# Performance work log

Measured on AMD Instinct MI355X. Metric: run time of the kernel, lower is better.

Reference implementation:

```python
import jax, jax.numpy as jnp
import numpy as np

N = 100000
CTX = 128
TGT = 32
H = 64
FUS = H + H // 2  # 96
E1 = 1600000
E2 = 800000
LN_EPS = 1e-5


def _gelu(x):
    return jax.nn.gelu(x, approximate=False)  # torch default is exact erf GELU


def _layer_norm(x, g, b):
    mu = jnp.mean(x, -1, keepdims=True)
    xc = x - mu
    var = jnp.mean(xc * xc, -1, keepdims=True)
    return xc * jax.lax.rsqrt(var + LN_EPS) * g + b


def _gcn_conv(x, W, b, ei, n):
    # PyG GCNConv: x' = D^-1/2 (A + I) D^-1/2 (x W) + b, with unit edge weights.
    h = x @ W  # [N, out]
    src, dst = ei[0], ei[1]
    deg = jnp.zeros((n,), h.dtype).at[dst].add(1.0) + 1.0  # +1 for self-loop
    dinv = jax.lax.rsqrt(deg)
    norm = dinv[src] * dinv[dst]  # [E]
    agg = jnp.zeros_like(h).at[dst].add(h[src] * norm[:, None])
    agg = agg + h * (dinv * dinv)[:, None]  # self-loop messages
    return agg + b


def setup_inputs() -> dict:
    key = jax.random.key(0)
    ks = jax.random.split(key, 32)
    def lin(k, fan_in, fan_out):
        s = 1.0 / np.sqrt(fan_in)
        k1, k2 = jax.random.split(k)
        return (jax.random.uniform(k1, (fan_in, fan_out), jnp.float32, -s, s),
                jax.random.uniform(k2, (fan_out,), jnp.float32, -s, s))
    inp = {}
    inp['context'] = jax.random.normal(ks[0], (N, CTX), jnp.float32)
    inp['target'] = jax.random.normal(ks[1], (N, TGT), jnp.float32)
    inp['mask'] = jax.random.bernoulli(ks[2], 0.5, (N, TGT))
    inp['adj_ei'] = jax.random.randint(ks[3], (2, E1), 0, N, jnp.int64 if jax.config.jax_enable_x64 else jnp.int32)
    inp['transit_ei'] = jax.random.randint(ks[4], (2, E2), 0, N, jnp.int64 if jax.config.jax_enable_x64 else jnp.int32)
    inp['mask_token'] = jax.random.normal(ks[5], (1, TGT), jnp.float32) * 0.01
    inp['ce_W1'], inp['ce_b1'] = lin(ks[6], CTX, H)
    inp['ce_g'] = jnp.ones((H,), jnp.float32)
    inp['ce_beta'] = jnp.zeros((H,), jnp.float32)
    inp['ce_W2'], inp['ce_b2'] = lin(ks[7], H, H)
    inp['te_W'], inp['te_b'] = lin(ks[8], TGT, H // 2)
    inp['g1_W'], inp['g1_b'] = lin(ks[9], FUS, H)
    inp['g2_W'], inp['g2_b'] = lin(ks[10], H, H)
    inp['t1_W'], inp['t1_b'] = lin(ks[11], FUS, H)
    inp['t2_W'], inp['t2_b'] = lin(ks[12], H, H)
    inp['alpha'] = jnp.float32(0.5)
    inp['h_W1'], inp['h_b1'] = lin(ks[13], H + FUS, H)
    inp['h_g'] = jnp.ones((H,), jnp.float32)
    inp['h_beta'] = jnp.zeros((H,), jnp.float32)
    inp['h_W2'], inp['h_b2'] = lin(ks[14], H, TGT)
    return inp


def reference(context, target, mask, adj_ei, transit_ei, mask_token,
              ce_W1, ce_b1, ce_g, ce_beta, ce_W2, ce_b2,
              te_W, te_b,
              g1_W, g1_b, g2_W, g2_b,
              t1_W, t1_b, t2_W, t2_b,
              alpha,
              h_W1, h_b1, h_g, h_beta, h_W2, h_b2):
    n = context.shape[0]
    # context encoder (eval mode: dropout is identity)
    c = _gelu(_layer_norm(context @ ce_W1 + ce_b1, ce_g, ce_beta))
    ctx = _gelu(c @ ce_W2 + ce_b2)
    # masked target encoder
    m = mask.astype(target.dtype)
    masked_t = target * (1.0 - m) + mask_token * m
    tgt = _gelu(masked_t @ te_W + te_b)
    fused = jnp.concatenate([ctx, tgt], -1)  # [N, 96]
    # spatial branch
    h1 = _gelu(_gcn_conv(fused, g1_W, g1_b, adj_ei, n))
    h_sp = _gcn_conv(h1, g2_W, g2_b, adj_ei, n)
    # transit branch
    h2 = _gelu(_gcn_conv(fused, t1_W, t1_b, transit_ei, n))
    h_tr = _gcn_conv(h2, t2_W, t2_b, transit_ei, n)
    a = jax.nn.sigmoid(alpha)
    h = a * h_sp + (1.0 - a) * h_tr
    z = jnp.concatenate([h, fused], -1)  # [N, 160]
    z = _gelu(_layer_norm(z @ h_W1 + h_b1, h_g, h_beta))
    return z @ h_W2 + h_b2  # [N, 32]
```

## Files before the change

kernel.cpp:

```cpp
#include <hip/hip_runtime.h>
#include <math.h>


#define LN_EPS 1e-5f
#define NRANGES 512
#define RMASK 511
#define LSHIFT 9
#define PASSP_EDGES 8192
#define GSTRIDE 16

typedef __attribute__((ext_vector_type(8))) short short8;
typedef __attribute__((ext_vector_type(4))) float float4v;
typedef __attribute__((ext_vector_type(4))) unsigned short ushort4v;

__device__ __forceinline__ float gelu_exact(float x) {
    return 0.5f * x * (1.0f + erff(x * 0.70710678118654752440f));
}

__device__ __forceinline__ float qsum16(float v) {
#pragma unroll
    for (int m = 1; m < 16; m <<= 1)
        v += __shfl_xor(v, m, 64);
    return v;
}

__device__ __forceinline__ int load_edge(const void* ei, int is32, long idx) {
    return is32 ? ((const int*)ei)[idx] : (int)((const long long*)ei)[idx];
}

__device__ __forceinline__ unsigned short f32_to_bf16(float f) {
    unsigned int x = __float_as_uint(f);
    x += 0x7fffu + ((x >> 16) & 1u);
    return (unsigned short)(x >> 16);
}
__device__ __forceinline__ float bf16_to_f32(unsigned short u) {
    return __uint_as_float((unsigned int)u << 16);
}
__device__ __forceinline__ float bflo(unsigned x) { return __uint_as_float(x << 16); }
__device__ __forceinline__ float bfhi(unsigned x) { return __uint_as_float(x & 0xffff0000u); }

__device__ __forceinline__ void load_dst4(const void* ei1, int e1, const void* ei2, int e2,
                                          int n, int is32, int base, int nv, int nd[4]) {
    if (is32 && nv == 4) {
        if (base + 3 < e1 && (((e1 + base) & 3) == 0)) {
            int4 v = *(const int4*)((const int*)ei1 + (size_t)e1 + base);
            nd[0] = v.x; nd[1] = v.y; nd[2] = v.z; nd[3] = v.w;
            return;
        }
        if (base >= e1 && (((e2 + base - e1) & 3) == 0)) {
            int4 v = *(const int4*)((const int*)ei2 + (size_t)e2 + (base - e1));
            nd[0] = v.x + n; nd[1] = v.y + n; nd[2] = v.z + n; nd[3] = v.w + n;
            return;
        }
    }
#pragma unroll
    for (int u = 0; u < 4; ++u) {
        int i = base + u;
        if (u >= nv) { nd[u] = -1; continue; }
        if (i < e1) nd[u] = load_edge(ei1, is32, (long)e1 + i);
        else        nd[u] = load_edge(ei2, is32, (long)e2 + (i - e1)) + n;
    }
}

__device__ __forceinline__ void load_src4(const void* ei1, int e1, const void* ei2, int e2,
                                          int is32, int base, int nv, int ns[4]) {
    if (is32 && nv == 4) {
        if (base + 3 < e1 && ((base & 3) == 0)) {
            int4 v = *(const int4*)((const int*)ei1 + base);
            ns[0] = v.x; ns[1] = v.y; ns[2] = v.z; ns[3] = v.w;
            return;
        }
        if (base >= e1 && (((base - e1) & 3) == 0)) {
            int4 v = *(const int4*)((const int*)ei2 + (base - e1));
            ns[0] = v.x; ns[1] = v.y; ns[2] = v.z; ns[3] = v.w;
            return;
        }
    }
#pragma unroll
    for (int u = 0; u < 4; ++u) {
        int i = base + u;
        if (u >= nv) { ns[u] = 0; continue; }
        if (i < e1) ns[u] = load_edge(ei1, is32, i);
        else        ns[u] = load_edge(ei2, is32, (long)(i - e1));
    }
}

__global__ __launch_bounds__(256) void detect_kernel(const unsigned char* __restrict__ mask_bytes,
                                                     const int* __restrict__ ei_words,
                                                     int* __restrict__ flags,
                                                     int* __restrict__ gcur, int cap) {
    if (blockIdx.x == 0) {
        __shared__ int f0, f1;
        if (threadIdx.x == 0) { f0 = 0; f1 = 0; }
        __syncthreads();
        int i = threadIdx.x;
        if ((i & 3) != 0 && mask_bytes[i] != 0) f0 = 1;
        if (i < 64 && ei_words[2 * i + 1] != 0) f1 = 1;
        __syncthreads();
        if (threadIdx.x == 0) { flags[0] = f0; flags[1] = f1; }
    } else {
        int r = (blockIdx.x - 1) * 256 + threadIdx.x;
        if (r < NRANGES) gcur[r * GSTRIDE] = r * cap;
    }
}

__device__ __forceinline__ void passp_body(
    const void* ei1, int e1, const void* ei2, int e2,
    int n, const int* flags, int* gcur, int cap, unsigned* ebuf, int sbits, int bid)
{
    __shared__ int hist[NRANGES];
    __shared__ int base[NRANGES];
    const int E = e1 + e2;
    const int is32 = flags[1];
    const int b0 = bid * PASSP_EDGES;
    const int bend = (b0 + PASSP_EDGES < E) ? b0 + PASSP_EDGES : E;
    const int tid = threadIdx.x;

    for (int k = tid; k < NRANGES; k += 1024) hist[k] = 0;
    __syncthreads();

    int nd[8], rk[8];
#pragma unroll
    for (int j = 0; j < 2; ++j) {
        int bi = b0 + j * 4096 + tid * 4;
        int nv = bend - bi; nv = (nv < 0) ? 0 : (nv > 4 ? 4 : nv);
        load_dst4(ei1, e1, ei2, e2, n, is32, bi, nv, &nd[j * 4]);
#pragma unroll
        for (int u = 0; u < 4; ++u)
            if (u < nv) rk[j * 4 + u] = atomicAdd(&hist[nd[j * 4 + u] & RMASK], 1);
    }
    __syncthreads();

    for (int r = tid; r < NRANGES; r += 1024) {
        int c = hist[r];
        base[r] = c ? atomicAdd(&gcur[r * GSTRIDE], c) : 0;
    }
    __syncthreads();

#pragma unroll
    for (int j = 0; j < 2; ++j) {
        int bi = b0 + j * 4096 + tid * 4;
        int nv = bend - bi; nv = (nv < 0) ? 0 : (nv > 4 ? 4 : nv);
        int sv[4];
        load_src4(ei1, e1, ei2, e2, is32, bi, nv, sv);
#pragma unroll
        for (int u = 0; u < 4; ++u) {
            if (u < nv) {
                int d = nd[j * 4 + u];
                int r = d & RMASK;
                int pos = base[r] + rk[j * 4 + u];
                if (pos < (r + 1) * cap)
                    ebuf[pos] = (unsigned)sv[u] | ((unsigned)(d >> LSHIFT) << sbits);
            }
        }
    }
}

__device__ __forceinline__ void prep_body(
    const float* context, const float* target, const void* mask, const int* flags,
    const float* mask_token, const float* te_W, const float* te_b,
    unsigned short* ctxb, unsigned short* fused, int n, int bid)
{
    __shared__ float tbuf[128][32];
    int w = threadIdx.x >> 6;
    int j = threadIdx.x & 63;
    int r0 = __builtin_amdgcn_readfirstlane(bid * 128 + w * 8);
    if (r0 >= n) return;

    const float4* src = (const float4*)(context + (size_t)r0 * 128);
    ushort4v* dst = (ushort4v*)(ctxb + (size_t)r0 * 128);
#pragma unroll
    for (int p = 0; p < 4; ++p) {
        float4 v = src[p * 64 + j];
        ushort4v o;
        o.x = f32_to_bf16(v.x); o.y = f32_to_bf16(v.y);
        o.z = f32_to_bf16(v.z); o.w = f32_to_bf16(v.w);
        dst[p * 64 + j] = o;
    }

    int tr = j >> 5;
    int tj = j & 31;
#pragma unroll
    for (int rr = 0; rr < 4; ++rr) {
        int r = tr + rr * 2;
        long mi = (long)(r0 + r) * 32 + tj;
        int mraw = flags[0] ? (int)((const unsigned char*)mask)[mi]
                            : ((const int*)mask)[mi];
        float m = mraw ? 1.0f : 0.0f;
        tbuf[w * 8 + r][tj] = target[mi] * (1.0f - m) + mask_token[tj] * m;
    }

#pragma unroll
    for (int rr = 0; rr < 4; ++rr) {
        int r = tr + rr * 2;
        float y3 = te_b[tj];
#pragma unroll
        for (int k = 0; k < 32; ++k)
            y3 = fmaf(tbuf[w * 8 + r][k], te_W[k * 32 + tj], y3);
        fused[(long)(r0 + r) * 96 + 64 + tj] = f32_to_bf16(gelu_exact(y3));
    }
}

__global__ __launch_bounds__(1024) void passp_prep_kernel(
    const void* __restrict__ ei1, int e1, const void* __restrict__ ei2, int e2,
    int n, const int* __restrict__ flags, int* __restrict__ gcur, int cap,
    unsigned* __restrict__ ebuf, int sbits, int ppBlocks,
    const float* __restrict__ context, const float* __restrict__ target,
    const void* __restrict__ mask, const float* __restrict__ mask_token,
    const float* __restrict__ te_W, const float* __restrict__ te_b,
    unsigned short* __restrict__ ctxb, unsigned short* __restrict__ fused)
{
    if ((int)blockIdx.x < ppBlocks)
        passp_body(ei1, e1, ei2, e2, n, flags, gcur, cap, ebuf, sbits, blockIdx.x);
    else
        prep_body(context, target, mask, flags, mask_token, te_W, te_b,
                  ctxb, fused, n, blockIdx.x - ppBlocks);
}

__device__ __forceinline__ void rscan_body(const int* gcur, int cap,
                                           int* rstart, int* rowptr, int n2) {
    __shared__ int ws[256];
    int t = threadIdx.x;
    int i0 = 2 * t, i1 = 2 * t + 1;
    int a0 = gcur[i0 * GSTRIDE] - i0 * cap;
    int a1 = gcur[i1 * GSTRIDE] - i1 * cap;
    ws[t] = a0 + a1;
    __syncthreads();
    for (int off = 1; off < 256; off <<= 1) {
        int v = (t >= off) ? ws[t - off] : 0;
        __syncthreads();
        if (t >= off) ws[t] += v;
        __syncthreads();
    }
    int ex = t ? ws[t - 1] : 0;
    rstart[i0] = ex;
    rstart[i1] = ex + a0;
    if (t == 255) { rstart[NRANGES] = ws[255]; rowptr[n2] = ws[255]; }
}

__device__ __forceinline__ void mfma_ln_body(
    const unsigned short* x, const float* W, const float* bias, const float* g,
    const float* beta, unsigned short* y, int n, int bid, int nblk)
{
    constexpr int K = 128, KS = K / 32, STRIDE = K + 8;
    __shared__ __align__(16) unsigned short wt[64 * STRIDE];
    int n0 = threadIdx.x & 63;
    int kk = threadIdx.x >> 6;
    for (int k = kk; k < K; k += 4)
        wt[n0 * STRIDE + k] = f32_to_bf16(W[k * 64 + n0]);
    __syncthreads();

    int w = threadIdx.x >> 6;
    int lane = threadIdx.x & 63;
    int c = lane & 15;
    int q = lane >> 4;

    short8 bfrag[KS][4];
#pragma unroll
    for (int s = 0; s < KS; ++s)
#pragma unroll
        for (int nt = 0; nt < 4; ++nt)
            bfrag[s][nt] = *(const short8*)&wt[(nt * 16 + c) * STRIDE + s * 32 + q * 8];

    float bs[4], gs[4], be[4];
#pragma unroll
    for (int nt = 0; nt < 4; ++nt) {
        bs[nt] = bias[nt * 16 + c];
        gs[nt] = g[nt * 16 + c];
        be[nt] = beta[nt * 16 + c];
    }

    int T = n >> 4;
    int stride = nblk * 4;
    for (int t = __builtin_amdgcn_readfirstlane(bid * 4 + w); t < T; t += stride) {
        int r0 = t << 4;
        const unsigned short* xa = x + (size_t)(r0 + c) * K + q * 8;
        float4v acc[4] = {{0,0,0,0},{0,0,0,0},{0,0,0,0},{0,0,0,0}};
#pragma unroll
        for (int s = 0; s < KS; ++s) {
            short8 a = *(const short8*)(xa + s * 32);
#pragma unroll
            for (int nt = 0; nt < 4; ++nt)
                acc[nt] = __builtin_amdgcn_mfma_f32_16x16x32_bf16(a, bfrag[s][nt], acc[nt], 0, 0, 0);
        }
#pragma unroll
        for (int reg = 0; reg < 4; ++reg) {
            float v0 = acc[0][reg] + bs[0];
            float v1 = acc[1][reg] + bs[1];
            float v2 = acc[2][reg] + bs[2];
            float v3 = acc[3][reg] + bs[3];
            float mean = qsum16((v0 + v1) + (v2 + v3)) * (1.0f / 64.0f);
            float x0 = v0 - mean, x1 = v1 - mean, x2 = v2 - mean, x3 = v3 - mean;
            float var = qsum16((x0 * x0 + x1 * x1) + (x2 * x2 + x3 * x3)) * (1.0f / 64.0f);
            float rstd = rsqrtf(var + LN_EPS);
            size_t row = (size_t)(r0 + q * 4 + reg) * 64;
            y[row + 0 * 16 + c] = f32_to_bf16(gelu_exact(x0 * rstd * gs[0] + be[0]));
            y[row + 1 * 16 + c] = f32_to_bf16(gelu_exact(x1 * rstd * gs[1] + be[1]));
            y[row + 2 * 16 + c] = f32_to_bf16(gelu_exact(x2 * rstd * gs[2] + be[2]));
            y[row + 3 * 16 + c] = f32_to_bf16(gelu_exact(x3 * rstd * gs[3] + be[3]));
        }
    }
}

__global__ __launch_bounds__(256) void ln_rscan_kernel(
    const unsigned short* __restrict__ x, const float* __restrict__ W,
    const float* __restrict__ bias, const float* __restrict__ g,
    const float* __restrict__ beta, unsigned short* __restrict__ y, int n, int nblk,
    const int* __restrict__ gcur, int cap, int* __restrict__ rstart,
    int* __restrict__ rowptr, int n2)
{
    if ((int)blockIdx.x == nblk)
        rscan_body(gcur, cap, rstart, rowptr, n2);
    else
        mfma_ln_body(x, W, bias, g, beta, y, n, blockIdx.x, nblk);
}

__device__ __forceinline__ void passq_body(
    const int* rstart, const unsigned* ebuf, int cap, int n2, int sbits,
    int* rowptr, int* rowcnt, float* dinv, int* srcs, int g)
{
    __shared__ int deg[NRANGES];
    __shared__ int cur[NRANGES];
    __shared__ int ws[256];
    const int t = threadIdx.x;
    const int gbase = rstart[g];
    const int total = rstart[g + 1] - gbase;
    const unsigned* eb = ebuf + (size_t)g * cap;
    const unsigned smask = (1u << sbits) - 1u;

    deg[2 * t] = 0; deg[2 * t + 1] = 0;
    __syncthreads();
    for (int i = t; i < total; i += 256)
        atomicAdd(&deg[eb[i] >> sbits], 1);
    __syncthreads();

    int a0 = deg[2 * t], a1 = deg[2 * t + 1];
    ws[t] = a0 + a1;
    __syncthreads();
    for (int off = 1; off < 256; off <<= 1) {
        int v = (t >= off) ? ws[t - off] : 0;
        __syncthreads();
        if (t >= off) ws[t] += v;
        __syncthreads();
    }
    int ex = t ? ws[t - 1] : 0;
    cur[2 * t] = ex;
    cur[2 * t + 1] = ex + a0;
    int node0 = ((2 * t) << LSHIFT) | g;
    int node1 = ((2 * t + 1) << LSHIFT) | g;
    if (node0 < n2) { rowptr[node0] = gbase + ex;      rowcnt[node0] = a0; dinv[node0] = rsqrtf((float)a0 + 1.0f); }
    if (node1 < n2) { rowptr[node1] = gbase + ex + a0; rowcnt[node1] = a1; dinv[node1] = rsqrtf((float)a1 + 1.0f); }
    __syncthreads();

    for (int i = t; i < total; i += 256) {
        unsigned e = eb[i];
        int rk = atomicAdd(&cur[e >> sbits], 1);
        srcs[gbase + rk] = (int)(e & smask);
    }
}

__device__ __forceinline__ void mfma_gelu_body(
    const unsigned short* x, const float* W, const float* bias,
    unsigned short* y, int n, int bid, int nblk)
{
    constexpr int K = 64, KS = K / 32, STRIDE = K + 8;
    __shared__ __align__(16) unsigned short wt[64 * STRIDE];
    int n0 = threadIdx.x & 63;
    int kk = threadIdx.x >> 6;
    for (int k = kk; k < K; k += 4)
        wt[n0 * STRIDE + k] = f32_to_bf16(W[k * 64 + n0]);
    __syncthreads();

    int w = threadIdx.x >> 6;
    int lane = threadIdx.x & 63;
    int c = lane & 15;
    int q = lane >> 4;

    short8 bfrag[KS][4];
#pragma unroll
    for (int s = 0; s < KS; ++s)
#pragma unroll
        for (int nt = 0; nt < 4; ++nt)
            bfrag[s][nt] = *(const short8*)&wt[(nt * 16 + c) * STRIDE + s * 32 + q * 8];

    float bs[4];
#pragma unroll
    for (int nt = 0; nt < 4; ++nt) bs[nt] = bias[nt * 16 + c];

    int T = n >> 4;
    int stride = nblk * 4;
    for (int t = __builtin_amdgcn_readfirstlane(bid * 4 + w); t < T; t += stride) {
        int r0 = t << 4;
        const unsigned short* xa = x + (size_t)(r0 + c) * K + q * 8;
        float4v acc[4] = {{0,0,0,0},{0,0,0,0},{0,0,0,0},{0,0,0,0}};
#pragma unroll
        for (int s = 0; s < KS; ++s) {
            short8 a = *(const short8*)(xa + s * 32);
#pragma unroll
            for (int nt = 0; nt < 4; ++nt)
                acc[nt] = __builtin_amdgcn_mfma_f32_16x16x32_bf16(a, bfrag[s][nt], acc[nt], 0, 0, 0);
        }
#pragma unroll
        for (int nt = 0; nt < 4; ++nt)
#pragma unroll
            for (int reg = 0; reg < 4; ++reg)
                y[(size_t)(r0 + q * 4 + reg) * 96 + nt * 16 + c] =
                    f32_to_bf16(gelu_exact(acc[nt][reg] + bs[nt]));
    }
}

__global__ __launch_bounds__(256) void passq_gelu_kernel(
    const int* __restrict__ rstart, const unsigned* __restrict__ ebuf, int cap, int n2,
    int sbits, int* __restrict__ rowptr, int* __restrict__ rowcnt,
    float* __restrict__ dinv, int* __restrict__ srcs,
    const unsigned short* __restrict__ x, const float* __restrict__ W,
    const float* __restrict__ bias, unsigned short* __restrict__ y, int n, int nblk)
{
    if ((int)blockIdx.x < NRANGES)
        passq_body(rstart, ebuf, cap, n2, sbits, rowptr, rowcnt, dinv, srcs, blockIdx.x);
    else
        mfma_gelu_body(x, W, bias, y, n, blockIdx.x - NRANGES, nblk);
}

__global__ __launch_bounds__(256) void mm_l1_dual_kernel(
    const unsigned short* __restrict__ x, const float* __restrict__ Wg,
    const float* __restrict__ Wt, const float* __restrict__ dinv,
    unsigned short* __restrict__ yg, unsigned short* __restrict__ yt, int n)
{
    constexpr int K = 96, KS = K / 32, STRIDE = K + 8;
    __shared__ __align__(16) unsigned short wtg[64 * STRIDE];
    __shared__ __align__(16) unsigned short wtt[64 * STRIDE];
    int n0 = threadIdx.x & 63;
    int kk = threadIdx.x >> 6;
    for (int k = kk; k < K; k += 4) {
        wtg[n0 * STRIDE + k] = f32_to_bf16(Wg[k * 64 + n0]);
        wtt[n0 * STRIDE + k] = f32_to_bf16(Wt[k * 64 + n0]);
    }
    __syncthreads();

    int w = threadIdx.x >> 6;
    int lane = threadIdx.x & 63;
    int c = lane & 15;
    int q = lane >> 4;

    short8 bg[KS][4], bt[KS][4];
#pragma unroll
    for (int s = 0; s < KS; ++s)
#pragma unroll
        for (int nt = 0; nt < 4; ++nt) {
            bg[s][nt] = *(const short8*)&wtg[(nt * 16 + c) * STRIDE + s * 32 + q * 8];
            bt[s][nt] = *(const short8*)&wtt[(nt * 16 + c) * STRIDE + s * 32 + q * 8];
        }

    int T = n >> 4;
    int stride = gridDim.x * 4;
    for (int t = __builtin_amdgcn_readfirstlane(blockIdx.x * 4 + w); t < T; t += stride) {
        int r0 = t << 4;
        const unsigned short* xa = x + (size_t)(r0 + c) * K + q * 8;
        float4v ag[4] = {{0,0,0,0},{0,0,0,0},{0,0,0,0},{0,0,0,0}};
        float4v at[4] = {{0,0,0,0},{0,0,0,0},{0,0,0,0},{0,0,0,0}};
#pragma unroll
        for (int s = 0; s < KS; ++s) {
            short8 a = *(const short8*)(xa + s * 32);
#pragma unroll
            for (int nt = 0; nt < 4; ++nt) {
                ag[nt] = __builtin_amdgcn_mfma_f32_16x16x32_bf16(a, bg[s][nt], ag[nt], 0, 0, 0);
                at[nt] = __builtin_amdgcn_mfma_f32_16x16x32_bf16(a, bt[s][nt], at[nt], 0, 0, 0);
            }
        }
        float sg[4], st[4];
#pragma unroll
        for (int reg = 0; reg < 4; ++reg) {
            sg[reg] = dinv[r0 + q * 4 + reg];
            st[reg] = dinv[n + r0 + q * 4 + reg];
        }
#pragma unroll
        for (int nt = 0; nt < 4; ++nt)
#pragma unroll
            for (int reg = 0; reg < 4; ++reg) {
                size_t row = (size_t)(r0 + q * 4 + reg) * 64 + nt * 16 + c;
                yg[row] = f32_to_bf16(ag[nt][reg] * sg[reg]);
                yt[row] = f32_to_bf16(at[nt][reg] * st[reg]);
            }
    }
}

__device__ __forceinline__ void mm64_body(const unsigned short* x, const float* W,
                                          const float* scale, unsigned short* y,
                                          int n, int bid, int nblk) {
    constexpr int K = 64, KS = K / 32, STRIDE = K + 8;
    __shared__ __align__(16) unsigned short wt[64 * STRIDE];
    int n0 = threadIdx.x & 63;
    int kk = threadIdx.x >> 6;
    for (int k = kk; k < K; k += 4)
        wt[n0 * STRIDE + k] = f32_to_bf16(W[k * 64 + n0]);
    __syncthreads();

    int w = threadIdx.x >> 6;
    int lane = threadIdx.x & 63;
    int c = lane & 15;
    int q = lane >> 4;

    short8 bfrag[KS][4];
#pragma unroll
    for (int s = 0; s < KS; ++s)
#pragma unroll
        for (int nt = 0; nt < 4; ++nt)
            bfrag[s][nt] = *(const short8*)&wt[(nt * 16 + c) * STRIDE + s * 32 + q * 8];

    int T = n >> 4;
    int stride = nblk * 4;
    for (int t = __builtin_amdgcn_readfirstlane(bid * 4 + w); t < T; t += stride) {
        int r0 = t << 4;
        const unsigned short* xa = x + (size_t)(r0 + c) * K + q * 8;
        float4v acc[4] = {{0,0,0,0},{0,0,0,0},{0,0,0,0},{0,0,0,0}};
#pragma unroll
        for (int s = 0; s < KS; ++s) {
            short8 a = *(const short8*)(xa + s * 32);
#pragma unroll
            for (int nt = 0; nt < 4; ++nt)
                acc[nt] = __builtin_amdgcn_mfma_f32_16x16x32_bf16(a, bfrag[s][nt], acc[nt], 0, 0, 0);
        }
        float sc[4];
#pragma unroll
        for (int reg = 0; reg < 4; ++reg)
            sc[reg] = scale[r0 + q * 4 + reg];
#pragma unroll
        for (int nt = 0; nt < 4; ++nt)
#pragma unroll
            for (int reg = 0; reg < 4; ++reg)
                y[(size_t)(r0 + q * 4 + reg) * 64 + nt * 16 + c] = f32_to_bf16(acc[nt][reg] * sc[reg]);
    }
}

__global__ __launch_bounds__(256) void mm_l2_kernel(
    const unsigned short* __restrict__ xg, const unsigned short* __restrict__ xt,
    const float* __restrict__ Wg, const float* __restrict__ Wt,
    const float* __restrict__ dinv,
    unsigned short* __restrict__ yg, unsigned short* __restrict__ yt, int n, int nblk)
{
    if ((int)blockIdx.x < nblk)
        mm64_body(xg, Wg, dinv, yg, n, blockIdx.x, nblk);
    else
        mm64_body(xt, Wt, dinv + n, yt, n, blockIdx.x - nblk, nblk);
}

__device__ __forceinline__ void gather4(const int* __restrict__ srcs,
                                        const unsigned short* __restrict__ lin,
                                        int beg, int cnt, int l, float acc[4]) {
    for (int base = 0; base < cnt; base += 16) {
        int c2 = cnt - base;
        if (c2 > 16) c2 = 16;
        int sj = (l < c2) ? srcs[beg + base + l] : 0;
        int t = 0;
        for (; t + 4 <= c2; t += 4) {
            uint2 v[4];
#pragma unroll
            for (int u = 0; u < 4; ++u) {
                int s = __shfl(sj, t + u, 16);
                v[u] = *(const uint2*)(lin + (size_t)((unsigned)s * 64u + (unsigned)(l * 4)));
            }
#pragma unroll
            for (int u = 0; u < 4; ++u) {
                acc[0] += bflo(v[u].x); acc[1] += bfhi(v[u].x);
                acc[2] += bflo(v[u].y); acc[3] += bfhi(v[u].y);
            }
        }
        for (; t < c2; ++t) {
            int s = __shfl(sj, t, 16);
            uint2 vv = *(const uint2*)(lin + (size_t)((unsigned)s * 64u + (unsigned)(l * 4)));
            acc[0] += bflo(vv.x); acc[1] += bfhi(vv.x);
            acc[2] += bflo(vv.y); acc[3] += bfhi(vv.y);
        }
    }
}

__global__ __launch_bounds__(256) void gather_l1_kernel(
    const int* __restrict__ rowptr, const int* __restrict__ rowcnt,
    const int* __restrict__ srcs, const float* __restrict__ dinv,
    const unsigned short* __restrict__ ling, const unsigned short* __restrict__ lint,
    const float* __restrict__ bg, const float* __restrict__ bt,
    unsigned short* __restrict__ h1g, unsigned short* __restrict__ h1t, int n)
{
    int w = threadIdx.x >> 6;
    int lane = threadIdx.x & 63;
    int g = lane >> 4;
    int l = lane & 15;
    int node = blockIdx.x * 16 + w * 4 + g;
    if (node >= n) return;

    float4 b4g = ((const float4*)bg)[l];
    float4 b4t = ((const float4*)bt)[l];
    unsigned off = (unsigned)node * 64u + (unsigned)(l * 4);

    {
        float acc[4] = {0, 0, 0, 0};
        gather4(srcs, ling, rowptr[node], rowcnt[node], l, acc);
        uint2 sv = *(const uint2*)(ling + off);
        acc[0] += bflo(sv.x); acc[1] += bfhi(sv.x);
        acc[2] += bflo(sv.y); acc[3] += bfhi(sv.y);
        float dd = dinv[node];
        ushort4v o;
        o.x = f32_to_bf16(gelu_exact(fmaf(dd, acc[0], b4g.x)));
        o.y = f32_to_bf16(gelu_exact(fmaf(dd, acc[1], b4g.y)));
        o.z = f32_to_bf16(gelu_exact(fmaf(dd, acc[2], b4g.z)));
        o.w = f32_to_bf16(gelu_exact(fmaf(dd, acc[3], b4g.w)));
        *(ushort4v*)(h1g + off) = o;
    }
    {
        int tn = n + node;
        float acc[4] = {0, 0, 0, 0};
        gather4(srcs, lint, rowptr[tn], rowcnt[tn], l, acc);
        uint2 sv = *(const uint2*)(lint + off);
        acc[0] += bflo(sv.x); acc[1] += bfhi(sv.x);
        acc[2] += bflo(sv.y); acc[3] += bfhi(sv.y);
        float dd = dinv[tn];
        ushort4v o;
        o.x = f32_to_bf16(gelu_exact(fmaf(dd, acc[0], b4t.x)));
        o.y = f32_to_bf16(gelu_exact(fmaf(dd, acc[1], b4t.y)));
        o.z = f32_to_bf16(gelu_exact(fmaf(dd, acc[2], b4t.z)));
        o.w = f32_to_bf16(gelu_exact(fmaf(dd, acc[3], b4t.w)));
        *(ushort4v*)(h1t + off) = o;
    }
}

__global__ __launch_bounds__(256) void gather_l2_kernel(
    const int* __restrict__ rowptr, const int* __restrict__ rowcnt,
    const int* __restrict__ srcs, const float* __restrict__ dinv,
    const unsigned short* __restrict__ ling, const unsigned short* __restrict__ lint,
    const float* __restrict__ bg, const float* __restrict__ bt,
    const float* __restrict__ alpha_ptr, unsigned short* __restrict__ hb, int n)
{
    int w = threadIdx.x >> 6;
    int lane = threadIdx.x & 63;
    int g = lane >> 4;
    int l = lane & 15;
    int node = blockIdx.x * 16 + w * 4 + g;
    if (node >= n) return;

    float4 b4g = ((const float4*)bg)[l];
    float4 b4t = ((const float4*)bt)[l];
    unsigned off = (unsigned)node * 64u + (unsigned)(l * 4);

    float pg[4], pt[4];
    {
        float acc[4] = {0, 0, 0, 0};
        gather4(srcs, ling, rowptr[node], rowcnt[node], l, acc);
        uint2 sv = *(const uint2*)(ling + off);
        acc[0] += bflo(sv.x); acc[1] += bfhi(sv.x);
        acc[2] += bflo(sv.y); acc[3] += bfhi(sv.y);
        float dd = dinv[node];
        pg[0] = fmaf(dd, acc[0], b4g.x); pg[1] = fmaf(dd, acc[1], b4g.y);
        pg[2] = fmaf(dd, acc[2], b4g.z); pg[3] = fmaf(dd, acc[3], b4g.w);
    }
    {
        int tn = n + node;
        float acc[4] = {0, 0, 0, 0};
        gather4(srcs, lint, rowptr[tn], rowcnt[tn], l, acc);
        uint2 sv = *(const uint2*)(lint + off);
        acc[0] += bflo(sv.x); acc[1] += bfhi(sv.x);
        acc[2] += bflo(sv.y); acc[3] += bfhi(sv.y);
        float dd = dinv[tn];
        pt[0] = fmaf(dd, acc[0], b4t.x); pt[1] = fmaf(dd, acc[1], b4t.y);
        pt[2] = fmaf(dd, acc[2], b4t.z); pt[3] = fmaf(dd, acc[3], b4t.w);
    }
    float a = 1.0f / (1.0f + expf(-alpha_ptr[0]));
    float b = 1.0f - a;
    ushort4v o;
    o.x = f32_to_bf16(a * pg[0] + b * pt[0]);
    o.y = f32_to_bf16(a * pg[1] + b * pt[1]);
    o.z = f32_to_bf16(a * pg[2] + b * pt[2]);
    o.w = f32_to_bf16(a * pg[3] + b * pt[3]);
    *(ushort4v*)(hb + off) = o;
}

__global__ __launch_bounds__(256) void head_mfma_kernel(
    const unsigned short* __restrict__ hb, const unsigned short* __restrict__ fused,
    const float* __restrict__ h_W1, const float* __restrict__ h_b1,
    const float* __restrict__ h_g, const float* __restrict__ h_beta,
    const float* __restrict__ h_W2, const float* __restrict__ h_b2,
    float* __restrict__ out, int n)
{
    constexpr int ST1 = 168;
    constexpr int ST2 = 72;
    __shared__ __align__(16) unsigned short wt1[64 * ST1];
    __shared__ __align__(16) unsigned short wt2[32 * ST2];
    __shared__ __align__(16) unsigned short zl[4][16 * ST2];

    int n0 = threadIdx.x & 63;
    int kk = threadIdx.x >> 6;
    for (int k = kk; k < 160; k += 4)
        wt1[n0 * ST1 + k] = f32_to_bf16(h_W1[k * 64 + n0]);
    if (n0 < 32)
        for (int k = kk; k < 64; k += 4)
            wt2[n0 * ST2 + k] = f32_to_bf16(h_W2[k * 32 + n0]);
    __syncthreads();

    int w = threadIdx.x >> 6;
    int lane = threadIdx.x & 63;
    int c = lane & 15;
    int q = lane >> 4;

    short8 b1f[5][4];
#pragma unroll
    for (int s = 0; s < 5; ++s)
#pragma unroll
        for (int nt = 0; nt < 4; ++nt)
            b1f[s][nt] = *(const short8*)&wt1[(nt * 16 + c) * ST1 + s * 32 + q * 8];
    short8 b2f[2][2];
#pragma unroll
    for (int s = 0; s < 2; ++s)
#pragma unroll
        for (int nt = 0; nt < 2; ++nt)
            b2f[s][nt] = *(const short8*)&wt2[(nt * 16 + c) * ST2 + s * 32 + q * 8];

    float bs[4], gs[4], be[4];
#pragma unroll
    for (int nt = 0; nt < 4; ++nt) {
        bs[nt] = h_b1[nt * 16 + c];
        gs[nt] = h_g[nt * 16 + c];
        be[nt] = h_beta[nt * 16 + c];
    }
    float b2s[2];
#pragma unroll
    for (int nt = 0; nt < 2; ++nt) b2s[nt] = h_b2[nt * 16 + c];

    unsigned short* zw = zl[w];
    int T = n >> 4;
    int stride = gridDim.x * 4;
    for (int t = __builtin_amdgcn_readfirstlane(blockIdx.x * 4 + w); t < T; t += stride) {
        int r0 = t << 4;
        const unsigned short* xh = hb + (size_t)(r0 + c) * 64 + q * 8;
        const unsigned short* xf = fused + (size_t)(r0 + c) * 96 + q * 8;
        float4v acc[4] = {{0,0,0,0},{0,0,0,0},{0,0,0,0},{0,0,0,0}};
#pragma unroll
        for (int s = 0; s < 2; ++s) {
            short8 a = *(const short8*)(xh + s * 32);
#pragma unroll
            for (int nt = 0; nt < 4; ++nt)
                acc[nt] = __builtin_amdgcn_mfma_f32_16x16x32_bf16(a, b1f[s][nt], acc[nt], 0, 0, 0);
        }
#pragma unroll
        for (int s = 0; s < 3; ++s) {
            short8 a = *(const short8*)(xf + s * 32);
#pragma unroll
            for (int nt = 0; nt < 4; ++nt)
                acc[nt] = __builtin_amdgcn_mfma_f32_16x16x32_bf16(a, b1f[2 + s][nt], acc[nt], 0, 0, 0);
        }
#pragma unroll
        for (int reg = 0; reg < 4; ++reg) {
            float v0 = acc[0][reg] + bs[0];
            float v1 = acc[1][reg] + bs[1];
            float v2 = acc[2][reg] + bs[2];
            float v3 = acc[3][reg] + bs[3];
            float mean = qsum16((v0 + v1) + (v2 + v3)) * (1.0f / 64.0f);
            float x0 = v0 - mean, x1 = v1 - mean, x2 = v2 - mean, x3 = v3 - mean;
            float var = qsum16((x0 * x0 + x1 * x1) + (x2 * x2 + x3 * x3)) * (1.0f / 64.0f);
            float rstd = rsqrtf(var + LN_EPS);
            int row = q * 4 + reg;
            zw[row * ST2 + 0 * 16 + c] = f32_to_bf16(gelu_exact(x0 * rstd * gs[0] + be[0]));
            zw[row * ST2 + 1 * 16 + c] = f32_to_bf16(gelu_exact(x1 * rstd * gs[1] + be[1]));
            zw[row * ST2 + 2 * 16 + c] = f32_to_bf16(gelu_exact(x2 * rstd * gs[2] + be[2]));
            zw[row * ST2 + 3 * 16 + c] = f32_to_bf16(gelu_exact(x3 * rstd * gs[3] + be[3]));
        }
        float4v acc2[2] = {{0,0,0,0},{0,0,0,0}};
#pragma unroll
        for (int s = 0; s < 2; ++s) {
            short8 a2 = *(const short8*)&zw[c * ST2 + s * 32 + q * 8];
#pragma unroll
            for (int nt = 0; nt < 2; ++nt)
                acc2[nt] = __builtin_amdgcn_mfma_f32_16x16x32_bf16(a2, b2f[s][nt], acc2[nt], 0, 0, 0);
        }
#pragma unroll
        for (int nt = 0; nt < 2; ++nt)
#pragma unroll
            for (int reg = 0; reg < 4; ++reg)
                out[(size_t)(r0 + q * 4 + reg) * 32 + nt * 16 + c] = acc2[nt][reg] + b2s[nt];
    }
}

extern "C" void kernel_launch(void* const* d_in, const int* in_sizes, int n_in,
                              void* d_out, int out_size, void* d_ws, size_t ws_size,
                              hipStream_t stream) {
    const float* context    = (const float*)d_in[0];
    const float* target     = (const float*)d_in[1];
    const void*  mask       = d_in[2];
    const void*  adj_ei     = d_in[3];
    const void*  tr_ei      = d_in[4];
    const float* mask_token = (const float*)d_in[5];
    const float* ce_W1 = (const float*)d_in[6];
    const float* ce_b1 = (const float*)d_in[7];
    const float* ce_g  = (const float*)d_in[8];
    const float* ce_be = (const float*)d_in[9];
    const float* ce_W2 = (const float*)d_in[10];
    const float* ce_b2 = (const float*)d_in[11];
    const float* te_W  = (const float*)d_in[12];
    const float* te_b  = (const float*)d_in[13];
    const float* g1_W  = (const float*)d_in[14];
    const float* g1_b  = (const float*)d_in[15];
    const float* g2_W  = (const float*)d_in[16];
    const float* g2_b  = (const float*)d_in[17];
    const float* t1_W  = (const float*)d_in[18];
    const float* t1_b  = (const float*)d_in[19];
    const float* t2_W  = (const float*)d_in[20];
    const float* t2_b  = (const float*)d_in[21];
    const float* alpha = (const float*)d_in[22];
    const float* h_W1  = (const float*)d_in[23];
    const float* h_b1  = (const float*)d_in[24];
    const float* h_g   = (const float*)d_in[25];
    const float* h_be  = (const float*)d_in[26];
    const float* h_W2  = (const float*)d_in[27];
    const float* h_b2  = (const float*)d_in[28];

    const int N  = in_sizes[0] / 128;
    const int E1 = in_sizes[3] / 2;
    const int E2 = in_sizes[4] / 2;
    const int E  = E1 + E2;
    const int N2 = 2 * N;

    int sbits = 1;
    while ((1 << sbits) < N) ++sbits;

    long expct = (E + NRANGES - 1) / NRANGES;
    int cap = (int)((expct * 4 / 3) & ~255L);
    long avail = (long)N * 128;
    int capmax = (int)((avail / ((long)NRANGES * 4)) & ~255L);
    if (cap > capmax) cap = capmax;
    if (cap < 1024) cap = 1024;

    char* p = (char*)d_ws;
    int*   flags  = (int*)p;                    p += 256;
    unsigned short* ctxb  = (unsigned short*)p; p += (size_t)N * 128 * 2;
    unsigned short* fused = (unsigned short*)p; p += (size_t)N * 96 * 2;
    unsigned short* cb    = (unsigned short*)p; p += (size_t)N * 64 * 2;
    unsigned short* lin   = (unsigned short*)p; p += (size_t)N * 64 * 2;
    unsigned short* h1    = (unsigned short*)p; p += (size_t)N * 64 * 2;
    unsigned short* hb    = (unsigned short*)p; p += (size_t)N * 64 * 2;
    float* hacc   = (float*)p;                  p += (size_t)N * 64 * 4;
    float* dinv   = (float*)p;                  p += (size_t)N2 * 4;
    int*   rowptr = (int*)p;                    p += (size_t)(N2 + 64) * 4;
    int*   rowcnt = (int*)p;                    p += (size_t)(N2 + 64) * 4;
    int*   gcur   = (int*)p;                    p += (size_t)NRANGES * GSTRIDE * 4;
    int*   rstart = (int*)p;                    p += (size_t)(NRANGES + 8) * 4;
    int*   srcs   = (int*)p;                    p += (size_t)E * 4;
    unsigned*       ebuf = (unsigned*)hacc;
    unsigned short* h1t  = (unsigned short*)((char*)hacc + (size_t)N * 128);
    unsigned short* h1g  = h1;
    unsigned short* ling = lin;
    unsigned short* lint = cb;
    float* out    = (float*)d_out;

    const unsigned prepBlocks   = (unsigned)((N + 127) / 128);
    const unsigned nodeBlocks16 = (unsigned)((N + 15) / 16);
    const unsigned ppBlocks     = (unsigned)((E + PASSP_EDGES - 1) / PASSP_EDGES);
    const unsigned mmBlocks     = 391;

    detect_kernel<<<3, 256, 0, stream>>>((const unsigned char*)mask, (const int*)adj_ei,
                                         flags, gcur, cap);
    passp_prep_kernel<<<ppBlocks + prepBlocks, 1024, 0, stream>>>(
        adj_ei, E1, tr_ei, E2, N, flags, gcur, cap, ebuf, sbits, (int)ppBlocks,
        context, target, mask, mask_token, te_W, te_b, ctxb, fused);
    ln_rscan_kernel<<<mmBlocks + 1, 256, 0, stream>>>(
        ctxb, ce_W1, ce_b1, ce_g, ce_be, cb, N, (int)mmBlocks,
        gcur, cap, rstart, rowptr, N2);
    passq_gelu_kernel<<<NRANGES + mmBlocks, 256, 0, stream>>>(
        rstart, ebuf, cap, N2, sbits, rowptr, rowcnt, dinv, srcs,
        cb, ce_W2, ce_b2, fused, N, (int)mmBlocks);

    mm_l1_dual_kernel<<<mmBlocks, 256, 0, stream>>>(fused, g1_W, t1_W, dinv, ling, lint, N);
    gather_l1_kernel<<<nodeBlocks16, 256, 0, stream>>>(rowptr, rowcnt, srcs, dinv,
                                                       ling, lint, g1_b, t1_b, h1g, h1t, N);
    mm_l2_kernel<<<2 * mmBlocks, 256, 0, stream>>>(h1g, h1t, g2_W, t2_W, dinv,
                                                   ling, lint, N, (int)mmBlocks);
    gather_l2_kernel<<<nodeBlocks16, 256, 0, stream>>>(rowptr, rowcnt, srcs, dinv,
                                                       ling, lint, g2_b, t2_b, alpha, hb, N);

    head_mfma_kernel<<<mmBlocks, 256, 0, stream>>>(hb, fused, h_W1, h_b1, h_g, h_be,
                                                   h_W2, h_b2, out, N);
}
```

Before: 401.2 us.

## Read fp32 context directly in LN matmul, drop bf16 staging copy; hoist src loads

The prep kernel no longer converts context to a bf16 staging buffer. The first LN+MFMA matmul now loads fp32 context rows and converts them to bf16 in registers. This removes one full write and one re-read of a 25 MB intermediate, at the cost of doubling the bytes read in the matmul. Separately, the edge partition pass loads source indices together with destination indices in its first phase, so they are held in registers across the sync instead of being reloaded.

Result: no change. 393.8 us (-1.8%).

```diff
diff --git a/kernel.cpp b/kernel.cpp
--- a/kernel.cpp
+++ b/kernel.cpp
@@ -119,12 +119,13 @@
     for (int k = tid; k < NRANGES; k += 1024) hist[k] = 0;
     __syncthreads();
 
-    int nd[8], rk[8];
+    int nd[8], rk[8], sv[8];
 #pragma unroll
     for (int j = 0; j < 2; ++j) {
         int bi = b0 + j * 4096 + tid * 4;
         int nv = bend - bi; nv = (nv < 0) ? 0 : (nv > 4 ? 4 : nv);
         load_dst4(ei1, e1, ei2, e2, n, is32, bi, nv, &nd[j * 4]);
+        load_src4(ei1, e1, ei2, e2, is32, bi, nv, &sv[j * 4]);
 #pragma unroll
         for (int u = 0; u < 4; ++u)
             if (u < nv) rk[j * 4 + u] = atomicAdd(&hist[nd[j * 4 + u] & RMASK], 1);
@@ -141,8 +142,6 @@
     for (int j = 0; j < 2; ++j) {
         int bi = b0 + j * 4096 + tid * 4;
         int nv = bend - bi; nv = (nv < 0) ? 0 : (nv > 4 ? 4 : nv);
-        int sv[4];
-        load_src4(ei1, e1, ei2, e2, is32, bi, nv, sv);
 #pragma unroll
         for (int u = 0; u < 4; ++u) {
             if (u < nv) {
@@ -150,33 +149,22 @@
                 int r = d & RMASK;
                 int pos = base[r] + rk[j * 4 + u];
                 if (pos < (r + 1) * cap)
-                    ebuf[pos] = (unsigned)sv[u] | ((unsigned)(d >> LSHIFT) << sbits);
+                    ebuf[pos] = (unsigned)sv[j * 4 + u] | ((unsigned)(d >> LSHIFT) << sbits);
             }
         }
     }
 }
 
 __device__ __forceinline__ void prep_body(
-    const float* context, const float* target, const void* mask, const int* flags,
+    const float* target, const void* mask, const int* flags,
     const float* mask_token, const float* te_W, const float* te_b,
-    unsigned short* ctxb, unsigned short* fused, int n, int bid)
+    unsigned short* fused, int n, int bid)
 {
     __shared__ float tbuf[128][32];
     int w = threadIdx.x >> 6;
     int j = threadIdx.x & 63;
     int r0 = __builtin_amdgcn_readfirstlane(bid * 128 + w * 8);
     if (r0 >= n) return;
-
-    const float4* src = (const float4*)(context + (size_t)r0 * 128);
-    ushort4v* dst = (ushort4v*)(ctxb + (size_t)r0 * 128);
-#pragma unroll
-    for (int p = 0; p < 4; ++p) {
-        float4 v = src[p * 64 + j];
-        ushort4v o;
-        o.x = f32_to_bf16(v.x); o.y = f32_to_bf16(v.y);
-        o.z = f32_to_bf16(v.z); o.w = f32_to_bf16(v.w);
-        dst[p * 64 + j] = o;
-    }
 
     int tr = j >> 5;
     int tj = j & 31;
@@ -205,16 +193,16 @@
     const void* __restrict__ ei1, int e1, const void* __restrict__ ei2, int e2,
     int n, const int* __restrict__ flags, int* __restrict__ gcur, int cap,
     unsigned* __restrict__ ebuf, int sbits, int ppBlocks,
-    const float* __restrict__ context, const float* __restrict__ target,
+    const float* __restrict__ target,
     const void* __restrict__ mask, const float* __restrict__ mask_token,
     const float* __restrict__ te_W, const float* __restrict__ te_b,
-    unsigned short* __restrict__ ctxb, unsigned short* __restrict__ fused)
+    unsigned short* __restrict__ fused)
 {
     if ((int)blockIdx.x < ppBlocks)
         passp_body(ei1, e1, ei2, e2, n, flags, gcur, cap, ebuf, sbits, blockIdx.x);
     else
-        prep_body(context, target, mask, flags, mask_token, te_W, te_b,
-                  ctxb, fused, n, blockIdx.x - ppBlocks);
+        prep_body(target, mask, flags, mask_token, te_W, te_b,
+                  fused, n, blockIdx.x - ppBlocks);
 }
 
 __device__ __forceinline__ void rscan_body(const int* gcur, int cap,
@@ -239,7 +227,7 @@
 }
 
 __device__ __forceinline__ void mfma_ln_body(
-    const unsigned short* x, const float* W, const float* bias, const float* g,
+    const float* x, const float* W, const float* bias, const float* g,
     const float* beta, unsigned short* y, int n, int bid, int nblk)
 {
     constexpr int K = 128, KS = K / 32, STRIDE = K + 8;
@@ -274,11 +262,17 @@
     int stride = nblk * 4;
     for (int t = __builtin_amdgcn_readfirstlane(bid * 4 + w); t < T; t += stride) {
         int r0 = t << 4;
-        const unsigned short* xa = x + (size_t)(r0 + c) * K + q * 8;
+        const float* xa = x + (size_t)(r0 + c) * K + q * 8;
         float4v acc[4] = {{0,0,0,0},{0,0,0,0},{0,0,0,0},{0,0,0,0}};
 #pragma unroll
         for (int s = 0; s < KS; ++s) {
-            short8 a = *(const short8*)(xa + s * 32);
+            float4 f0 = *(const float4*)(xa + s * 32);
+            float4 f1 = *(const float4*)(xa + s * 32 + 4);
+            short8 a;
+            a[0] = (short)f32_to_bf16(f0.x); a[1] = (short)f32_to_bf16(f0.y);
+            a[2] = (short)f32_to_bf16(f0.z); a[3] = (short)f32_to_bf16(f0.w);
+            a[4] = (short)f32_to_bf16(f1.x); a[5] = (short)f32_to_bf16(f1.y);
+            a[6] = (short)f32_to_bf16(f1.z); a[7] = (short)f32_to_bf16(f1.w);
 #pragma unroll
             for (int nt = 0; nt < 4; ++nt)
                 acc[nt] = __builtin_amdgcn_mfma_f32_16x16x32_bf16(a, bfrag[s][nt], acc[nt], 0, 0, 0);
@@ -303,7 +297,7 @@
 }
 
 __global__ __launch_bounds__(256) void ln_rscan_kernel(
-    const unsigned short* __restrict__ x, const float* __restrict__ W,
+    const float* __restrict__ x, const float* __restrict__ W,
     const float* __restrict__ bias, const float* __restrict__ g,
     const float* __restrict__ beta, unsigned short* __restrict__ y, int n, int nblk,
     const int* __restrict__ gcur, int cap, int* __restrict__ rstart,
@@ -830,7 +824,6 @@
 
     char* p = (char*)d_ws;
     int*   flags  = (int*)p;                    p += 256;
-    unsigned short* ctxb  = (unsigned short*)p; p += (size_t)N * 128 * 2;
     unsigned short* fused = (unsigned short*)p; p += (size_t)N * 96 * 2;
     unsigned short* cb    = (unsigned short*)p; p += (size_t)N * 64 * 2;
     unsigned short* lin   = (unsigned short*)p; p += (size_t)N * 64 * 2;
@@ -859,9 +852,9 @@
                                          flags, gcur, cap);
     passp_prep_kernel<<<ppBlocks + prepBlocks, 1024, 0, stream>>>(
         adj_ei, E1, tr_ei, E2, N, flags, gcur, cap, ebuf, sbits, (int)ppBlocks,
-        context, target, mask, mask_token, te_W, te_b, ctxb, fused);
+        target, mask, mask_token, te_W, te_b, fused);
     ln_rscan_kernel<<<mmBlocks + 1, 256, 0, stream>>>(
-        ctxb, ce_W1, ce_b1, ce_g, ce_be, cb, N, (int)mmBlocks,
+        context, ce_W1, ce_b1, ce_g, ce_be, cb, N, (int)mmBlocks,
         gcur, cap, rstart, rowptr, N2);
     passq_gelu_kernel<<<NRANGES + mmBlocks, 256, 0, stream>>>(
         rstart, ebuf, cap, N2, sbits, rowptr, rowcnt, dinv, srcs,
```
